# Performance work log

Hardware: AMD Instinct MI355X
Metric: run time of the kernel (lower is better)

## Reference

```python
import jax, jax.numpy as jnp
import numpy as np

N_NODES = 50000
N_EDGES = 800000


def _inv_sqrt_deg(idx, n):
    deg = jax.ops.segment_sum(jnp.ones(idx.shape, jnp.float32), idx, num_segments=n)
    return jnp.where(deg > 0, deg ** -0.5, 0.0)


def graph_conv(x, W, b, src, dst, norm_src, norm_dst):
    # DGL GraphConv, norm='both': D_dst^{-1/2} A D_src^{-1/2} X W + b
    # Apply weight before aggregation (out_feats < in_feats in both layers).
    h = (x * norm_src[:, None]) @ W            # [N, out]
    m = h[src]                                  # gather per-edge messages [E, out]
    agg = jax.ops.segment_sum(m, dst, num_segments=x.shape[0])
    return agg * norm_dst[:, None] + b


def setup_inputs() -> dict:
    key = jax.random.key(0)
    ks = jax.random.split(key, 6)
    x = jax.random.normal(ks[0], (N_NODES, 512), jnp.float32)
    W1 = jax.random.normal(ks[1], (512, 128), jnp.float32) * (512 ** -0.5)
    b1 = jnp.zeros((128,), jnp.float32)
    W2 = jax.random.normal(ks[2], (128, 40), jnp.float32) * (128 ** -0.5)
    b2 = jnp.zeros((40,), jnp.float32)
    src = jax.random.randint(ks[3], (N_EDGES,), 0, N_NODES, jnp.int32)
    dst = jax.random.randint(ks[4], (N_EDGES,), 0, N_NODES, jnp.int32)
    return {"x": x, "W1": W1, "b1": b1, "W2": W2, "b2": b2, "src": src, "dst": dst}


def reference(x, W1, b1, W2, b2, src, dst):
    n = x.shape[0]
    norm_src = _inv_sqrt_deg(src, n)  # out-degree based src norm
    norm_dst = _inv_sqrt_deg(dst, n)  # in-degree based dst norm
    h = graph_conv(x, W1, b1, src, dst, norm_src, norm_dst)
    h = jax.nn.relu(h)
    h = graph_conv(h, W2, b2, src, dst, norm_src, norm_dst)
    return h
```

## Files before the change

### kernel.cpp

```cpp
#include <hip/hip_runtime.h>
#include <hip/hip_bf16.h>

#define F0 512
#define F1 128
#define F2 40

#define NRP 12800
#define G_SL 64

typedef __attribute__((ext_vector_type(8))) short bf16x8;
typedef __attribute__((ext_vector_type(4))) float f32x4;

__device__ inline ushort f2bf(float f) {
    union { float f; uint u; } v; v.f = f;
    uint u = v.u;
    uint r = u + 0x7fffu + ((u >> 16) & 1u);
    return (ushort)(r >> 16);
}

__global__ __launch_bounds__(1024)
void hist_kernel(const int* __restrict__ src, const int* __restrict__ dst,
                 ushort* __restrict__ Gsrc, ushort* __restrict__ Gdst,
                 const float* __restrict__ W1, ushort* __restrict__ Wt, int n, int E) {
    if (blockIdx.x < (F0 * F1) / 1024) {
        int idx = blockIdx.x * 1024 + threadIdx.x;
        int k = idx >> 7, nn = idx & 127;
        Wt[nn * F0 + k] = f2bf(W1[idx]);
    }
    __shared__ uint cs[NRP / 2];
    __shared__ uint cd[NRP / 2];
    const int p = blockIdx.x / G_SL;
    const int g = blockIdx.x % G_SL;
    const int base = p * NRP;
    for (int i = threadIdx.x; i < NRP / 2; i += 1024) { cs[i] = 0; cd[i] = 0; }
    __syncthreads();
    const int Epg = (E + G_SL - 1) / G_SL;
    const int e0 = g * Epg;
    const int e1 = min(E, e0 + Epg);
    for (int i = e0 + (int)threadIdx.x; i < e1; i += 1024) {
        int s = src[i], d = dst[i];
        unsigned so = (unsigned)(s - base);
        unsigned dd = (unsigned)(d - base);
        if (so < (unsigned)NRP) atomicAdd(&cs[so >> 1], 1u << ((so & 1) * 16));
        if (dd < (unsigned)NRP) atomicAdd(&cd[dd >> 1], 1u << ((dd & 1) * 16));
    }
    __syncthreads();
    const int lim = min(NRP, n - base);
    for (int i = threadIdx.x; i < lim; i += 1024) {
        uint pcs = cs[i >> 1], pcd = cd[i >> 1];
        int sh = (i & 1) * 16;
        Gsrc[(size_t)g * n + base + i] = (ushort)((pcs >> sh) & 0xffffu);
        Gdst[(size_t)g * n + base + i] = (ushort)((pcd >> sh) & 0xffffu);
    }
}

__global__ __launch_bounds__(256)
void scanA_kernel(const ushort* __restrict__ Gsrc, const ushort* __restrict__ Gdst,
                  float* __restrict__ norm_src, float* __restrict__ norm_dst,
                  int* __restrict__ row_off, int* __restrict__ bsum, int n) {
    __shared__ int sm[256];
    int i = blockIdx.x * 256 + threadIdx.x;
    int s = 0, d = 0;
    if (i < n) {
#pragma unroll
        for (int g = 0; g < G_SL; g++) {
            s += Gsrc[(size_t)g * n + i];
            d += Gdst[(size_t)g * n + i];
        }
        norm_src[i] = s > 0 ? rsqrtf((float)s) : 0.f;
        norm_dst[i] = d > 0 ? rsqrtf((float)d) : 0.f;
    }
    sm[threadIdx.x] = (i < n) ? d : 0;
    __syncthreads();
    for (int off = 1; off < 256; off <<= 1) {
        int t = (threadIdx.x >= (unsigned)off) ? sm[threadIdx.x - off] : 0;
        __syncthreads();
        sm[threadIdx.x] += t;
        __syncthreads();
    }
    if (i < n) row_off[i + 1] = sm[threadIdx.x];
    if (threadIdx.x == 255) bsum[blockIdx.x] = sm[255];
}

__global__ __launch_bounds__(256)
void finalize_kernel(int* __restrict__ row_off, const int* __restrict__ bsum,
                     const ushort* __restrict__ Gdst, int* __restrict__ Goff, int n) {
    __shared__ int sm[256];
    const int b = blockIdx.x;
    const int t = threadIdx.x;
    sm[t] = (t < b) ? bsum[t] : 0;
    __syncthreads();
#pragma unroll
    for (int off = 128; off > 0; off >>= 1) {
        if (t < off) sm[t] += sm[t + off];
        __syncthreads();
    }
    const int excl = sm[0];
    const int v = b * 256 + t;
    if (v >= n) return;
    int raw = row_off[v];
    int start = excl + ((t == 0) ? 0 : raw);
    if (v == n - 1) {
        int rawn = row_off[n];
        row_off[n] = excl + rawn;
    }
    row_off[v] = start;
    int run = start;
#pragma unroll
    for (int g = 0; g < G_SL; g++) {
        size_t idx = (size_t)g * n + v;
        Goff[idx] = run;
        run += Gdst[idx];
    }
}

__global__ __launch_bounds__(1024)
void place_kernel(const int* __restrict__ src, const int* __restrict__ dst,
                  const int* __restrict__ Goff, int* __restrict__ edge_src, int n, int E) {
    __shared__ int cur[NRP];
    const int p = blockIdx.x / G_SL;
    const int g = blockIdx.x % G_SL;
    const int base = p * NRP;
    const int lim = min(NRP, n - base);
    for (int i = threadIdx.x; i < lim; i += 1024)
        cur[i] = Goff[(size_t)g * n + base + i];
    __syncthreads();
    const int Epg = (E + G_SL - 1) / G_SL;
    const int e0 = g * Epg;
    const int e1 = min(E, e0 + Epg);
    for (int i = e0 + (int)threadIdx.x; i < e1; i += 1024) {
        int d = dst[i];
        unsigned dd = (unsigned)(d - base);
        if (dd < (unsigned)lim) {
            int pos = atomicAdd(&cur[dd], 1);
            edge_src[pos] = src[i];
        }
    }
}

#define BM 64
__global__ __launch_bounds__(256)
void gemm1_mfma(const float* __restrict__ x, const ushort* __restrict__ Wt,
                const float* __restrict__ norm_src, ushort* __restrict__ h1g, int n) {
    __shared__ __align__(16) ushort Al[2][4][64][8];

    const int tid = threadIdx.x;
    const int lane = tid & 63;
    const int w = tid >> 6;
    const int l15 = lane & 15;
    const int lq = lane >> 4;
    const int bm = blockIdx.x * BM;

    const int smi = tid >> 6;
    const int sflane = tid & 63;
    const int srow = smi * 16 + (tid & 15);
    const int skc = (tid >> 4) & 3;
    const int grow = bm + srow;
    const bool arok = grow < n;
    const float* xrow = x + (size_t)(arok ? grow : 0) * F0 + skc * 8;

    const size_t bg0 = (size_t)((w * 2 + 0) * 16 + l15) * F0 + lq * 8;
    const size_t bg1 = (size_t)((w * 2 + 1) * 16 + l15) * F0 + lq * 8;

    f32x4 acc[4][2] = {};
    float4 sa0, sa1;
    float4 sb0, sb1;
    bf16x8 bcur0, bcur1, bnxt0, bnxt1;

    auto loadA_A = [&](int k0) {
        if (arok) {
            sa0 = *reinterpret_cast<const float4*>(xrow + k0);
            sa1 = *reinterpret_cast<const float4*>(xrow + k0 + 4);
        } else { sa0 = make_float4(0.f, 0.f, 0.f, 0.f); sa1 = sa0; }
    };
    auto loadA_B = [&](int k0) {
        if (arok) {
            sb0 = *reinterpret_cast<const float4*>(xrow + k0);
            sb1 = *reinterpret_cast<const float4*>(xrow + k0 + 4);
        } else { sb0 = make_float4(0.f, 0.f, 0.f, 0.f); sb1 = sb0; }
    };
    auto stage = [&](int buf, const float4& c0, const float4& c1) {
        float cf[8] = {c0.x, c0.y, c0.z, c0.w, c1.x, c1.y, c1.z, c1.w};
        uint hu[4];
#pragma unroll
        for (int j = 0; j < 4; j++) {
            __hip_bfloat162 h2 = __float22bfloat162_rn(make_float2(cf[2 * j], cf[2 * j + 1]));
            __builtin_memcpy(&hu[j], &h2, 4);
        }
        *reinterpret_cast<uint4*>(&Al[buf][smi][sflane][0]) = make_uint4(hu[0], hu[1], hu[2], hu[3]);
    };
    auto loadB = [&](int k0, bf16x8& b0, bf16x8& b1) {
        b0 = *reinterpret_cast<const bf16x8*>(Wt + bg0 + k0);
        b1 = *reinterpret_cast<const bf16x8*>(Wt + bg1 + k0);
    };
    auto compute = [&](int buf, bf16x8 b0, bf16x8 b1) {
#pragma unroll
        for (int mi = 0; mi < 4; mi++) {
            bf16x8 a = *reinterpret_cast<const bf16x8*>(&Al[buf][mi][lane][0]);
            acc[mi][0] = __builtin_amdgcn_mfma_f32_16x16x32_bf16(a, b0, acc[mi][0], 0, 0, 0);
            acc[mi][1] = __builtin_amdgcn_mfma_f32_16x16x32_bf16(a, b1, acc[mi][1], 0, 0, 0);
        }
    };

    loadA_A(0);
    loadA_B(32);
    loadB(0, bcur0, bcur1);
    stage(0, sa0, sa1);
    __syncthreads();

#pragma unroll
    for (int kt = 0; kt < 16; kt++) {
        const int cb = kt & 1;
        if (kt < 14) {
            if ((kt & 1) == 0) loadA_A((kt + 2) * 32);
            else               loadA_B((kt + 2) * 32);
        }
        if (kt < 15) loadB((kt + 1) * 32, bnxt0, bnxt1);
        compute(cb, bcur0, bcur1);
        if (kt < 15) {
            if (((kt + 1) & 1) == 0) stage(cb ^ 1, sa0, sa1);
            else                     stage(cb ^ 1, sb0, sb1);
            bcur0 = bnxt0; bcur1 = bnxt1;
            __syncthreads();
        }
    }

#pragma unroll
    for (int mi = 0; mi < 4; mi++) {
        int rbase = bm + mi * 16 + lq * 4;
#pragma unroll
        for (int r = 0; r < 4; r++) {
            int row = rbase + r;
            if (row < n) {
                float ns = norm_src[row];
#pragma unroll
                for (int ni = 0; ni < 2; ni++) {
                    h1g[(size_t)row * F1 + w * 32 + ni * 16 + l15] = f2bf(acc[mi][ni][r] * ns);
                }
            }
        }
    }
}

__global__ __launch_bounds__(256)
void agg1_kernel(const ushort* __restrict__ h1g, const int* __restrict__ row_off,
                 const int* __restrict__ edge_src, const float* __restrict__ norm_dst,
                 const float* __restrict__ b1, ushort* __restrict__ h1, int n) {
    int wid = (blockIdx.x * blockDim.x + threadIdx.x) >> 6;
    int lane = threadIdx.x & 63;
    if (wid >= n) return;
    int beg = row_off[wid], end = row_off[wid + 1];
    float a0 = 0.f, a1 = 0.f;
    int e = beg;
    for (; e + 7 < end; e += 8) {
        int s[8];
#pragma unroll
        for (int j = 0; j < 8; j++) s[j] = edge_src[e + j];
        uint v[8];
#pragma unroll
        for (int j = 0; j < 8; j++)
            v[j] = *reinterpret_cast<const uint*>(&h1g[(size_t)s[j] * F1 + lane * 2]);
#pragma unroll
        for (int j = 0; j < 8; j++) {
            a0 += __uint_as_float(v[j] << 16);
            a1 += __uint_as_float(v[j] & 0xffff0000u);
        }
    }
    for (; e < end; ++e) {
        int s = edge_src[e];
        uint v = *reinterpret_cast<const uint*>(&h1g[(size_t)s * F1 + lane * 2]);
        a0 += __uint_as_float(v << 16);
        a1 += __uint_as_float(v & 0xffff0000u);
    }
    float nd = norm_dst[wid];
    float o0 = fmaxf(a0 * nd + b1[lane * 2 + 0], 0.f);
    float o1 = fmaxf(a1 * nd + b1[lane * 2 + 1], 0.f);
    __hip_bfloat162 p2 = __float22bfloat162_rn(make_float2(o0, o1));
    uint pu; __builtin_memcpy(&pu, &p2, 4);
    *reinterpret_cast<uint*>(&h1[(size_t)wid * F1 + lane * 2]) = pu;
}

__global__ __launch_bounds__(256)
void gemm2_kernel(const ushort* __restrict__ h1, const float* __restrict__ W2,
                  const float* __restrict__ norm_src, ushort* __restrict__ h2g, int n) {
    __shared__ __align__(16) float W2s[F1][F2];
    for (int i = threadIdx.x; i < F1 * F2; i += 256)
        W2s[i / F2][i % F2] = W2[i];
    __syncthreads();
    int node = blockIdx.x * 256 + threadIdx.x;
    if (node >= n) return;
    float nrm = norm_src[node];
    f32x4 acc4[10] = {};
    const ushort* row = &h1[(size_t)node * F1];
    for (int kc = 0; kc < 16; kc++) {
        uint4 u = *reinterpret_cast<const uint4*>(&row[kc * 8]);
        uint uu[4] = {u.x, u.y, u.z, u.w};
        float f[8];
#pragma unroll
        for (int i = 0; i < 4; i++) {
            f[2 * i + 0] = __uint_as_float(uu[i] << 16);
            f[2 * i + 1] = __uint_as_float(uu[i] & 0xffff0000u);
        }
#pragma unroll
        for (int j = 0; j < 8; j++) {
#pragma unroll
            for (int c4 = 0; c4 < 10; c4++) {
                f32x4 wv = *reinterpret_cast<const f32x4*>(&W2s[kc * 8 + j][c4 * 4]);
                acc4[c4] += f[j] * wv;
            }
        }
    }
    ushort* orow = &h2g[(size_t)node * F2];
#pragma unroll
    for (int c4 = 0; c4 < 10; c4++) {
        f32x4 o = acc4[c4] * nrm;
        __hip_bfloat162 pa = __float22bfloat162_rn(make_float2(o[0], o[1]));
        __hip_bfloat162 pb = __float22bfloat162_rn(make_float2(o[2], o[3]));
        uint2 pk;
        __builtin_memcpy(&pk.x, &pa, 4);
        __builtin_memcpy(&pk.y, &pb, 4);
        *reinterpret_cast<uint2*>(&orow[c4 * 4]) = pk;
    }
}

__global__ __launch_bounds__(256)
void agg2_kernel(const ushort* __restrict__ h2g, const int* __restrict__ row_off,
                 const int* __restrict__ edge_src, const float* __restrict__ norm_dst,
                 const float* __restrict__ b2, float* __restrict__ out, int n) {
    int wid = (blockIdx.x * blockDim.x + threadIdx.x) >> 6;
    int lane = threadIdx.x & 63;
    if (wid >= n) return;
    int beg = row_off[wid], end = row_off[wid + 1];
    float a0 = 0.f, a1 = 0.f;
    int e = beg;
    const bool act = lane < 20;
    for (; e + 7 < end; e += 8) {
        int s[8];
#pragma unroll
        for (int j = 0; j < 8; j++) s[j] = edge_src[e + j];
        if (act) {
            uint v[8];
#pragma unroll
            for (int j = 0; j < 8; j++)
                v[j] = *reinterpret_cast<const uint*>(&h2g[(size_t)s[j] * F2 + lane * 2]);
#pragma unroll
            for (int j = 0; j < 8; j++) {
                a0 += __uint_as_float(v[j] << 16);
                a1 += __uint_as_float(v[j] & 0xffff0000u);
            }
        }
    }
    for (; e < end; ++e) {
        int s = edge_src[e];
        if (act) {
            uint v = *reinterpret_cast<const uint*>(&h2g[(size_t)s * F2 + lane * 2]);
            a0 += __uint_as_float(v << 16);
            a1 += __uint_as_float(v & 0xffff0000u);
        }
    }
    if (act) {
        float nd = norm_dst[wid];
        float o0 = a0 * nd + b2[lane * 2 + 0];
        float o1 = a1 * nd + b2[lane * 2 + 1];
        *reinterpret_cast<float2*>(&out[(size_t)wid * F2 + lane * 2]) = make_float2(o0, o1);
    }
}

extern "C" void kernel_launch(void* const* d_in, const int* in_sizes, int n_in,
                              void* d_out, int out_size, void* d_ws, size_t ws_size,
                              hipStream_t stream) {
    const float* x  = (const float*)d_in[0];
    const float* W1 = (const float*)d_in[1];
    const float* b1 = (const float*)d_in[2];
    const float* W2 = (const float*)d_in[3];
    const float* b2 = (const float*)d_in[4];
    const int* src  = (const int*)d_in[5];
    const int* dst  = (const int*)d_in[6];
    float* out = (float*)d_out;

    const int n = in_sizes[0] / F0;
    const int E = in_sizes[5];
    const int nb = (n + 255) / 256;
    const int P = (n + NRP - 1) / NRP;

    char* ws = (char*)d_ws;
    auto alloc = [&](size_t bytes) -> char* {
        char* p = ws;
        ws += (bytes + 255) & ~(size_t)255;
        return p;
    };
    int* row_off   = (int*)alloc((size_t)(n + 1) * 4);
    int* bsum      = (int*)alloc(256 * 4);
    int* edge_srcs = (int*)alloc((size_t)E * 4);
    float* norm_src_d = (float*)alloc((size_t)n * 4);
    float* norm_dst_d = (float*)alloc((size_t)n * 4);
    ushort* W1t = (ushort*)alloc((size_t)F1 * F0 * 2);
    ushort* h1g = (ushort*)alloc((size_t)n * F1 * 2);
    ushort* h1  = (ushort*)alloc((size_t)n * F1 * 2);
    ushort* h2g = h1g;

    ushort* Gsrc = (ushort*)h1g;
    ushort* Gdst = Gsrc + (size_t)G_SL * n;
    int* Goff = (int*)h1;

    hist_kernel<<<P * G_SL, 1024, 0, stream>>>(src, dst, Gsrc, Gdst, W1, W1t, n, E);
    scanA_kernel<<<nb, 256, 0, stream>>>(Gsrc, Gdst, norm_src_d, norm_dst_d, row_off, bsum, n);
    finalize_kernel<<<nb, 256, 0, stream>>>(row_off, bsum, Gdst, Goff, n);
    place_kernel<<<P * G_SL, 1024, 0, stream>>>(src, dst, Goff, edge_srcs, n, E);
    gemm1_mfma<<<(n + BM - 1) / BM, 256, 0, stream>>>(x, W1t, norm_src_d, h1g, n);
    agg1_kernel<<<(n + 3) / 4, 256, 0, stream>>>(h1g, row_off, edge_srcs, norm_dst_d, b1, h1, n);
    gemm2_kernel<<<(n + 255) / 256, 256, 0, stream>>>(h1, W2, norm_src_d, h2g, n);
    agg2_kernel<<<(n + 3) / 4, 256, 0, stream>>>(h2g, row_off, edge_srcs, norm_dst_d, b2, out, n);
}
```

Measured before the change: 192.5 us.

## Pre-convert x to bf16 in hist kernel and simplify gemm1 to register-resident A

Converts the fp32 input features to a bf16 buffer inside the histogram kernel via a grid-stride loop. gemm1 then reads bf16 directly, with each wave keeping its 16-row A slice in registers and computing all 128 output columns, reading W from cache and using no LDS staging or barriers. This removes per-tile conversion and synchronisation in the GEMM but adds a full extra write and read of a half-size copy of x, plus a large workspace buffer.

```diff
diff --git a/kernel.cpp b/kernel.cpp
--- a/kernel.cpp
+++ b/kernel.cpp
@@ -18,14 +18,29 @@
     return (ushort)(r >> 16);
 }
 
+#define CVT2(dst, a, b) { __hip_bfloat162 _t2 = __float22bfloat162_rn(make_float2(a, b)); __builtin_memcpy(&dst, &_t2, 4); }
+
 __global__ __launch_bounds__(1024)
 void hist_kernel(const int* __restrict__ src, const int* __restrict__ dst,
                  ushort* __restrict__ Gsrc, ushort* __restrict__ Gdst,
-                 const float* __restrict__ W1, ushort* __restrict__ Wt, int n, int E) {
+                 const float* __restrict__ W1, ushort* __restrict__ Wt,
+                 const float* __restrict__ x, ushort* __restrict__ xb, int n, int E) {
     if (blockIdx.x < (F0 * F1) / 1024) {
         int idx = blockIdx.x * 1024 + threadIdx.x;
         int k = idx >> 7, nn = idx & 127;
         Wt[nn * F0 + k] = f2bf(W1[idx]);
+    }
+    {
+        const int total = n * (F0 / 8);
+        const int stride = gridDim.x * 1024;
+        for (int i = blockIdx.x * 1024 + threadIdx.x; i < total; i += stride) {
+            float4 p0 = *reinterpret_cast<const float4*>(x + (size_t)i * 8);
+            float4 p1 = *reinterpret_cast<const float4*>(x + (size_t)i * 8 + 4);
+            uint h0, h1, h2, h3;
+            CVT2(h0, p0.x, p0.y); CVT2(h1, p0.z, p0.w);
+            CVT2(h2, p1.x, p1.y); CVT2(h3, p1.z, p1.w);
+            *reinterpret_cast<uint4*>(xb + (size_t)i * 8) = make_uint4(h0, h1, h2, h3);
+        }
     }
     __shared__ uint cs[NRP / 2];
     __shared__ uint cd[NRP / 2];
@@ -140,103 +155,45 @@
 
 #define BM 64
 __global__ __launch_bounds__(256)
-void gemm1_mfma(const float* __restrict__ x, const ushort* __restrict__ Wt,
+void gemm1_mfma(const ushort* __restrict__ xb, const ushort* __restrict__ Wt,
                 const float* __restrict__ norm_src, ushort* __restrict__ h1g, int n) {
-    __shared__ __align__(16) ushort Al[2][4][64][8];
-
     const int tid = threadIdx.x;
     const int lane = tid & 63;
     const int w = tid >> 6;
     const int l15 = lane & 15;
     const int lq = lane >> 4;
-    const int bm = blockIdx.x * BM;
-
-    const int smi = tid >> 6;
-    const int sflane = tid & 63;
-    const int srow = smi * 16 + (tid & 15);
-    const int skc = (tid >> 4) & 3;
-    const int grow = bm + srow;
-    const bool arok = grow < n;
-    const float* xrow = x + (size_t)(arok ? grow : 0) * F0 + skc * 8;
-
-    const size_t bg0 = (size_t)((w * 2 + 0) * 16 + l15) * F0 + lq * 8;
-    const size_t bg1 = (size_t)((w * 2 + 1) * 16 + l15) * F0 + lq * 8;
-
-    f32x4 acc[4][2] = {};
-    float4 sa0, sa1;
-    float4 sb0, sb1;
-    bf16x8 bcur0, bcur1, bnxt0, bnxt1;
-
-    auto loadA_A = [&](int k0) {
-        if (arok) {
-            sa0 = *reinterpret_cast<const float4*>(xrow + k0);
-            sa1 = *reinterpret_cast<const float4*>(xrow + k0 + 4);
-        } else { sa0 = make_float4(0.f, 0.f, 0.f, 0.f); sa1 = sa0; }
-    };
-    auto loadA_B = [&](int k0) {
-        if (arok) {
-            sb0 = *reinterpret_cast<const float4*>(xrow + k0);
-            sb1 = *reinterpret_cast<const float4*>(xrow + k0 + 4);
-        } else { sb0 = make_float4(0.f, 0.f, 0.f, 0.f); sb1 = sb0; }
-    };
-    auto stage = [&](int buf, const float4& c0, const float4& c1) {
-        float cf[8] = {c0.x, c0.y, c0.z, c0.w, c1.x, c1.y, c1.z, c1.w};
-        uint hu[4];
-#pragma unroll
-        for (int j = 0; j < 4; j++) {
-            __hip_bfloat162 h2 = __float22bfloat162_rn(make_float2(cf[2 * j], cf[2 * j + 1]));
-            __builtin_memcpy(&hu[j], &h2, 4);
-        }
-        *reinterpret_cast<uint4*>(&Al[buf][smi][sflane][0]) = make_uint4(hu[0], hu[1], hu[2], hu[3]);
-    };
-    auto loadB = [&](int k0, bf16x8& b0, bf16x8& b1) {
-        b0 = *reinterpret_cast<const bf16x8*>(Wt + bg0 + k0);
-        b1 = *reinterpret_cast<const bf16x8*>(Wt + bg1 + k0);
-    };
-    auto compute = [&](int buf, bf16x8 b0, bf16x8 b1) {
-#pragma unroll
-        for (int mi = 0; mi < 4; mi++) {
-            bf16x8 a = *reinterpret_cast<const bf16x8*>(&Al[buf][mi][lane][0]);
-            acc[mi][0] = __builtin_amdgcn_mfma_f32_16x16x32_bf16(a, b0, acc[mi][0], 0, 0, 0);
-            acc[mi][1] = __builtin_amdgcn_mfma_f32_16x16x32_bf16(a, b1, acc[mi][1], 0, 0, 0);
-        }
-    };
-
-    loadA_A(0);
-    loadA_B(32);
-    loadB(0, bcur0, bcur1);
-    stage(0, sa0, sa1);
-    __syncthreads();
+    const int rbase = blockIdx.x * BM + w * 16;
+
+    const int arow = rbase + l15;
+    const ushort* xrow = xb + (size_t)(arow < n ? arow : 0) * F0 + lq * 8;
+
+    bf16x8 a[16];
+#pragma unroll
+    for (int kt = 0; kt < 16; kt++)
+        a[kt] = *reinterpret_cast<const bf16x8*>(xrow + kt * 32);
+
+    const ushort* bp = Wt + (size_t)l15 * F0 + lq * 8;
+    f32x4 acc[8] = {};
 
 #pragma unroll
     for (int kt = 0; kt < 16; kt++) {
-        const int cb = kt & 1;
-        if (kt < 14) {
-            if ((kt & 1) == 0) loadA_A((kt + 2) * 32);
-            else               loadA_B((kt + 2) * 32);
-        }
-        if (kt < 15) loadB((kt + 1) * 32, bnxt0, bnxt1);
-        compute(cb, bcur0, bcur1);
-        if (kt < 15) {
-            if (((kt + 1) & 1) == 0) stage(cb ^ 1, sa0, sa1);
-            else                     stage(cb ^ 1, sb0, sb1);
-            bcur0 = bnxt0; bcur1 = bnxt1;
-            __syncthreads();
-        }
-    }
-
-#pragma unroll
-    for (int mi = 0; mi < 4; mi++) {
-        int rbase = bm + mi * 16 + lq * 4;
-#pragma unroll
-        for (int r = 0; r < 4; r++) {
-            int row = rbase + r;
-            if (row < n) {
-                float ns = norm_src[row];
-#pragma unroll
-                for (int ni = 0; ni < 2; ni++) {
-                    h1g[(size_t)row * F1 + w * 32 + ni * 16 + l15] = f2bf(acc[mi][ni][r] * ns);
-                }
+        bf16x8 b[8];
+#pragma unroll
+        for (int ni = 0; ni < 8; ni++)
+            b[ni] = *reinterpret_cast<const bf16x8*>(bp + (size_t)ni * 16 * F0 + kt * 32);
+#pragma unroll
+        for (int ni = 0; ni < 8; ni++)
+            acc[ni] = __builtin_amdgcn_mfma_f32_16x16x32_bf16(a[kt], b[ni], acc[ni], 0, 0, 0);
+    }
+
+#pragma unroll
+    for (int r = 0; r < 4; r++) {
+        int orow = rbase + lq * 4 + r;
+        if (orow < n) {
+            float ns = norm_src[orow];
+#pragma unroll
+            for (int ni = 0; ni < 8; ni++) {
+                h1g[(size_t)orow * F1 + ni * 16 + l15] = f2bf(acc[ni][r] * ns);
             }
         }
     }
@@ -395,6 +352,7 @@
     float* norm_src_d = (float*)alloc((size_t)n * 4);
     float* norm_dst_d = (float*)alloc((size_t)n * 4);
     ushort* W1t = (ushort*)alloc((size_t)F1 * F0 * 2);
+    ushort* xb  = (ushort*)alloc((size_t)n * F0 * 2);
     ushort* h1g = (ushort*)alloc((size_t)n * F1 * 2);
     ushort* h1  = (ushort*)alloc((size_t)n * F1 * 2);
     ushort* h2g = h1g;
@@ -403,11 +361,11 @@
     ushort* Gdst = Gsrc + (size_t)G_SL * n;
     int* Goff = (int*)h1;
 
-    hist_kernel<<<P * G_SL, 1024, 0, stream>>>(src, dst, Gsrc, Gdst, W1, W1t, n, E);
+    hist_kernel<<<P * G_SL, 1024, 0, stream>>>(src, dst, Gsrc, Gdst, W1, W1t, x, xb, n, E);
     scanA_kernel<<<nb, 256, 0, stream>>>(Gsrc, Gdst, norm_src_d, norm_dst_d, row_off, bsum, n);
     finalize_kernel<<<nb, 256, 0, stream>>>(row_off, bsum, Gdst, Goff, n);
     place_kernel<<<P * G_SL, 1024, 0, stream>>>(src, dst, Goff, edge_srcs, n, E);
-    gemm1_mfma<<<(n + BM - 1) / BM, 256, 0, stream>>>(x, W1t, norm_src_d, h1g, n);
+    gemm1_mfma<<<(n + BM - 1) / BM, 256, 0, stream>>>(xb, W1t, norm_src_d, h1g, n);
     agg1_kernel<<<(n + 3) / 4, 256, 0, stream>>>(h1g, row_off, edge_srcs, norm_dst_d, b1, h1, n);
     gemm2_kernel<<<(n + 255) / 256, 256, 0, stream>>>(h1, W2, norm_src_d, h2g, n);
     agg2_kernel<<<(n + 3) / 4, 256, 0, stream>>>(h2g, row_off, edge_srcs, norm_dst_d, b2, out, n);
```

After: 236.2 us. +22.7%, slower.
